# Kernel tuning notes

Measured on AMD Instinct MI355X. Metric: run time of the kernel, lower is better.

Reference implementation:

```python
import jax, jax.numpy as jnp
import numpy as np

EMBED, HEADS, FF, WIN = 512, 8, 2048, 64
SIGMA, PSTRENGTH, PERIOD, THRESH = 2.0, 1.0, 100.0, 0.0


def layer_norm(x, g, b, eps=1e-5):
    mu = jnp.mean(x, axis=-1, keepdims=True)
    var = jnp.var(x, axis=-1, keepdims=True)
    return (x - mu) * jax.lax.rsqrt(var + eps) * g + b


def setup_inputs() -> dict:
    key = jax.random.key(0)
    ks = jax.random.split(key, 16)
    s = 1.0 / np.sqrt(EMBED)
    sf = 1.0 / np.sqrt(FF)
    inp = {
        "src": jax.random.normal(ks[0], (8, 2048, EMBED), dtype=jnp.float32),
        "Wq": jax.random.normal(ks[1], (EMBED, EMBED), dtype=jnp.float32) * s,
        "bq": jnp.zeros((EMBED,), jnp.float32),
        "Wk": jax.random.normal(ks[2], (EMBED, EMBED), dtype=jnp.float32) * s,
        "bk": jnp.zeros((EMBED,), jnp.float32),
        "Wv": jax.random.normal(ks[3], (EMBED, EMBED), dtype=jnp.float32) * s,
        "bv": jnp.zeros((EMBED,), jnp.float32),
        "Wo": jax.random.normal(ks[4], (EMBED, EMBED), dtype=jnp.float32) * s,
        "bo": jnp.zeros((EMBED,), jnp.float32),
        "Wg": jax.random.normal(ks[5], (EMBED, 1), dtype=jnp.float32) * s,
        "bg": jnp.zeros((1,), jnp.float32),
        "W1": jax.random.normal(ks[6], (EMBED, FF), dtype=jnp.float32) * s,
        "b1": jnp.zeros((FF,), jnp.float32),
        "W2": jax.random.normal(ks[7], (FF, EMBED), dtype=jnp.float32) * sf,
        "b2": jnp.zeros((EMBED,), jnp.float32),
        "ln1_g": jnp.ones((EMBED,), jnp.float32),
        "ln1_b": jnp.zeros((EMBED,), jnp.float32),
        "ln2_g": jnp.ones((EMBED,), jnp.float32),
        "ln2_b": jnp.zeros((EMBED,), jnp.float32),
    }
    return inp


def gated_sparse_attn(x, Wq, bq, Wk, bk, Wv, bv, Wo, bo, Wg, bg):
    B, S, D = x.shape
    H, dh = HEADS, D // HEADS
    q = (x @ Wq + bq).reshape(B, S, H, dh).transpose(0, 2, 1, 3)  # [B,H,S,dh]
    k = (x @ Wk + bk).reshape(B, S, H, dh).transpose(0, 2, 1, 3)
    v = (x @ Wv + bv).reshape(B, S, H, dh).transpose(0, 2, 1, 3)
    scores = jnp.einsum('bhqd,bhkd->bhqk', q, k) / jnp.sqrt(jnp.float32(dh))
    idx = jnp.arange(S, dtype=jnp.float32)
    dist = idx[:, None] - idx[None, :]  # [S,S]
    gauss_bias = jnp.exp(-(dist * dist) / (2.0 * SIGMA * SIGMA))
    per_bias = PSTRENGTH * jnp.cos(2.0 * jnp.pi * dist / PERIOD)
    scores = scores + gauss_bias + per_bias  # positional biases baked into scores
    local = jnp.abs(dist) <= WIN  # local-window sparsity mask
    scores = jnp.where(local, scores, jnp.float32(-1e9))
    attn = jax.nn.softmax(scores, axis=-1)
    out = jnp.einsum('bhqk,bhkd->bhqd', attn, v)
    out = out.transpose(0, 2, 1, 3).reshape(B, S, D) @ Wo + bo
    gate = jax.nn.sigmoid(x @ Wg + bg)  # [B,S,1] learned gating
    gate = jnp.where(gate > THRESH, gate, jnp.float32(0.0))
    return gate * out


def reference(src, Wq, bq, Wk, bk, Wv, bv, Wo, bo, Wg, bg, W1, b1, W2, b2, ln1_g, ln1_b, ln2_g, ln2_b):
    # dropout is identity in eval mode
    attn_out = gated_sparse_attn(src, Wq, bq, Wk, bk, Wv, bv, Wo, bo, Wg, bg)
    x = layer_norm(src + attn_out, ln1_g, ln1_b)
    ff = jax.nn.relu(x @ W1 + b1) @ W2 + b2
    return layer_norm(x + ff, ln2_g, ln2_b)
```

## Files before the change

### kernel.cpp

```cpp
#include <hip/hip_runtime.h>
#include <hip/hip_bf16.h>
#include <math.h>

#define S_LEN   2048
#define D_MOD   512
#define N_HEADS 8
#define D_HEAD  64
#define FF_DIM  2048
#define M_ROWS  16384
#define BHSD    8388608

typedef __attribute__((ext_vector_type(8))) __bf16 bf16x8;
typedef __attribute__((ext_vector_type(4))) float  f32x4;
typedef unsigned short u16;

__device__ __forceinline__ u16 f2bf(float f) {
  unsigned u = __float_as_uint(f);
  u += 0x7fffu + ((u >> 16) & 1u);
  return (u16)(u >> 16);
}
__device__ __forceinline__ float bf2f(u16 h) { return __uint_as_float(((unsigned)h) << 16); }

__device__ __forceinline__ f32x4 mfma16(bf16x8 a, bf16x8 b, f32x4 c) {
  return __builtin_amdgcn_mfma_f32_16x16x32_bf16(a, b, c, 0, 0, 0);
}

__device__ __forceinline__ void async16(void* lds, const void* g) {
  __builtin_amdgcn_global_load_lds(
      (const __attribute__((address_space(1))) unsigned int*)g,
      (__attribute__((address_space(3))) unsigned int*)lds, 16, 0, 0);
}

#define BAR()    asm volatile("s_barrier" ::: "memory")
#define WAITV(n) asm volatile("s_waitcnt vmcnt(" #n ")" ::: "memory")
#define WAITL()  asm volatile("s_waitcnt lgkmcnt(0)" ::: "memory")

__device__ __forceinline__ int swz384(int row, int bir) {
  return row * 384 + ((bir & ~127) | ((bir ^ ((row & 7) << 4)) & 127));
}

__global__ __launch_bounds__(256) void cvt_gate(const float* __restrict__ src,
                                                const float* __restrict__ Wg,
                                                const float* __restrict__ bg,
                                                u16* __restrict__ xb,
                                                float* __restrict__ gate) {
  const int wid = threadIdx.x >> 6, lane = threadIdx.x & 63;
  const size_t row = (size_t)blockIdx.x * 4 + wid;
  const float4* s = reinterpret_cast<const float4*>(src + row * D_MOD);
  const float4* w = reinterpret_cast<const float4*>(Wg);
  float4 a0 = s[lane * 2], a1 = s[lane * 2 + 1];
  float4 w0 = w[lane * 2], w1 = w[lane * 2 + 1];
  float acc = a0.x * w0.x + a0.y * w0.y + a0.z * w0.z + a0.w * w0.w +
              a1.x * w1.x + a1.y * w1.y + a1.z * w1.z + a1.w * w1.w;
#pragma unroll
  for (int m = 1; m < 64; m <<= 1) acc += __shfl_xor(acc, m);
  ushort4 h0, h1;
  h0.x = f2bf(a0.x); h0.y = f2bf(a0.y); h0.z = f2bf(a0.z); h0.w = f2bf(a0.w);
  h1.x = f2bf(a1.x); h1.y = f2bf(a1.y); h1.z = f2bf(a1.z); h1.w = f2bf(a1.w);
  ushort4* ob = reinterpret_cast<ushort4*>(xb + row * D_MOD);
  ob[lane * 2] = h0; ob[lane * 2 + 1] = h1;
  if (lane == 0) {
    float g = 1.f / (1.f + __expf(-(acc + bg[0])));
    gate[row] = g > 0.f ? g : 0.f;
  }
}

__global__ void transpose_cvt(const float* __restrict__ in, u16* __restrict__ out,
                              int K, int N) {
  __shared__ float t[32][33];
  const int n0 = blockIdx.x * 32, k0 = blockIdx.y * 32;
  const int tx = threadIdx.x, ty = threadIdx.y;
#pragma unroll
  for (int i = 0; i < 4; ++i)
    t[ty + 8 * i][tx] = in[(size_t)(k0 + ty + 8 * i) * N + n0 + tx];
  __syncthreads();
#pragma unroll
  for (int i = 0; i < 4; ++i)
    out[(size_t)(n0 + ty + 8 * i) * K + k0 + tx] = f2bf(t[tx][ty + 8 * i]);
}

__global__ __launch_bounds__(256) void ln1red_k(const u16* __restrict__ xb,
                                                const float* __restrict__ gate,
                                                const u16* __restrict__ p0,
                                                const u16* __restrict__ p1,
                                                const float* __restrict__ bo,
                                                const float* __restrict__ gam,
                                                const float* __restrict__ bet,
                                                u16* __restrict__ outb) {
  const int wid = threadIdx.x >> 6, lane = threadIdx.x & 63;
  const size_t row = (size_t)blockIdx.x * 4 + wid;
  const size_t base = row * D_MOD;
  const float g = gate[row];
  const ushort4* sp = reinterpret_cast<const ushort4*>(xb + base);
  const ushort4* a  = reinterpret_cast<const ushort4*>(p0 + base);
  const ushort4* c  = reinterpret_cast<const ushort4*>(p1 + base);
  const float4*  bb = reinterpret_cast<const float4*>(bo);
  ushort4 s0 = sp[lane * 2], s1 = sp[lane * 2 + 1];
  ushort4 a0 = a[lane * 2], a1 = a[lane * 2 + 1];
  ushort4 c0 = c[lane * 2], c1 = c[lane * 2 + 1];
  float4 d0 = bb[lane * 2], d1 = bb[lane * 2 + 1];
  float4 v0, v1;
  v0.x = bf2f(s0.x) + g * (bf2f(a0.x) + bf2f(c0.x) + d0.x);
  v0.y = bf2f(s0.y) + g * (bf2f(a0.y) + bf2f(c0.y) + d0.y);
  v0.z = bf2f(s0.z) + g * (bf2f(a0.z) + bf2f(c0.z) + d0.z);
  v0.w = bf2f(s0.w) + g * (bf2f(a0.w) + bf2f(c0.w) + d0.w);
  v1.x = bf2f(s1.x) + g * (bf2f(a1.x) + bf2f(c1.x) + d1.x);
  v1.y = bf2f(s1.y) + g * (bf2f(a1.y) + bf2f(c1.y) + d1.y);
  v1.z = bf2f(s1.z) + g * (bf2f(a1.z) + bf2f(c1.z) + d1.z);
  v1.w = bf2f(s1.w) + g * (bf2f(a1.w) + bf2f(c1.w) + d1.w);
  float s  = v0.x + v0.y + v0.z + v0.w + v1.x + v1.y + v1.z + v1.w;
  float s2 = v0.x * v0.x + v0.y * v0.y + v0.z * v0.z + v0.w * v0.w +
             v1.x * v1.x + v1.y * v1.y + v1.z * v1.z + v1.w * v1.w;
#pragma unroll
  for (int m = 1; m < 64; m <<= 1) { s += __shfl_xor(s, m); s2 += __shfl_xor(s2, m); }
  const float mu = s * (1.0f / 512.0f);
  const float var = s2 * (1.0f / 512.0f) - mu * mu;
  const float rs = 1.0f / sqrtf(var + 1e-5f);
  const float4* gp = reinterpret_cast<const float4*>(gam);
  const float4* bp = reinterpret_cast<const float4*>(bet);
  float4 g0 = gp[lane * 2], g1 = gp[lane * 2 + 1];
  float4 e0 = bp[lane * 2], e1 = bp[lane * 2 + 1];
  ushort4 h0, h1;
  h0.x = f2bf((v0.x - mu) * rs * g0.x + e0.x);  h0.y = f2bf((v0.y - mu) * rs * g0.y + e0.y);
  h0.z = f2bf((v0.z - mu) * rs * g0.z + e0.z);  h0.w = f2bf((v0.w - mu) * rs * g0.w + e0.w);
  h1.x = f2bf((v1.x - mu) * rs * g1.x + e1.x);  h1.y = f2bf((v1.y - mu) * rs * g1.y + e1.y);
  h1.z = f2bf((v1.z - mu) * rs * g1.z + e1.z);  h1.w = f2bf((v1.w - mu) * rs * g1.w + e1.w);
  ushort4* ob = reinterpret_cast<ushort4*>(outb + base);
  ob[lane * 2] = h0; ob[lane * 2 + 1] = h1;
}

__global__ __launch_bounds__(256) void ln2red_k(const u16* __restrict__ xb,
                                                const u16* __restrict__ p0,
                                                const u16* __restrict__ p1,
                                                const float* __restrict__ b2,
                                                const float* __restrict__ gam,
                                                const float* __restrict__ bet,
                                                float* __restrict__ out) {
  const int wid = threadIdx.x >> 6, lane = threadIdx.x & 63;
  const size_t row = (size_t)blockIdx.x * 4 + wid;
  const size_t base = row * D_MOD;
  const ushort4* xp = reinterpret_cast<const ushort4*>(xb + base);
  const ushort4* q0 = reinterpret_cast<const ushort4*>(p0 + base);
  const ushort4* q1 = reinterpret_cast<const ushort4*>(p1 + base);
  const float4* bb = reinterpret_cast<const float4*>(b2);
  ushort4 h0 = xp[lane * 2], h1 = xp[lane * 2 + 1];
  ushort4 a0 = q0[lane * 2], a1 = q0[lane * 2 + 1];
  ushort4 c0 = q1[lane * 2], c1 = q1[lane * 2 + 1];
  float4 d0 = bb[lane * 2], d1 = bb[lane * 2 + 1];
  float4 v0, v1;
  v0.x = bf2f(h0.x) + bf2f(a0.x) + bf2f(c0.x) + d0.x;
  v0.y = bf2f(h0.y) + bf2f(a0.y) + bf2f(c0.y) + d0.y;
  v0.z = bf2f(h0.z) + bf2f(a0.z) + bf2f(c0.z) + d0.z;
  v0.w = bf2f(h0.w) + bf2f(a0.w) + bf2f(c0.w) + d0.w;
  v1.x = bf2f(h1.x) + bf2f(a1.x) + bf2f(c1.x) + d1.x;
  v1.y = bf2f(h1.y) + bf2f(a1.y) + bf2f(c1.y) + d1.y;
  v1.z = bf2f(h1.z) + bf2f(a1.z) + bf2f(c1.z) + d1.z;
  v1.w = bf2f(h1.w) + bf2f(a1.w) + bf2f(c1.w) + d1.w;
  float s  = v0.x + v0.y + v0.z + v0.w + v1.x + v1.y + v1.z + v1.w;
  float s2 = v0.x * v0.x + v0.y * v0.y + v0.z * v0.z + v0.w * v0.w +
             v1.x * v1.x + v1.y * v1.y + v1.z * v1.z + v1.w * v1.w;
#pragma unroll
  for (int m = 1; m < 64; m <<= 1) { s += __shfl_xor(s, m); s2 += __shfl_xor(s2, m); }
  const float mu = s * (1.0f / 512.0f);
  const float var = s2 * (1.0f / 512.0f) - mu * mu;
  const float rs = 1.0f / sqrtf(var + 1e-5f);
  const float4* gp = reinterpret_cast<const float4*>(gam);
  const float4* bp = reinterpret_cast<const float4*>(bet);
  float4 g0 = gp[lane * 2], g1 = gp[lane * 2 + 1];
  float4 e0 = bp[lane * 2], e1 = bp[lane * 2 + 1];
  float4 o0, o1;
  o0.x = (v0.x - mu) * rs * g0.x + e0.x;  o0.y = (v0.y - mu) * rs * g0.y + e0.y;
  o0.z = (v0.z - mu) * rs * g0.z + e0.z;  o0.w = (v0.w - mu) * rs * g0.w + e0.w;
  o1.x = (v1.x - mu) * rs * g1.x + e1.x;  o1.y = (v1.y - mu) * rs * g1.y + e1.y;
  o1.z = (v1.z - mu) * rs * g1.z + e1.z;  o1.w = (v1.w - mu) * rs * g1.w + e1.w;
  float4* q = reinterpret_cast<float4*>(out + base);
  q[lane * 2] = o0; q[lane * 2 + 1] = o1;
}

struct EpiArgs {
  const float* b0; const float* b1; const float* b2;
  float* outf; u16* outb; u16* outb2;
};

template<int EPI, int LD, int NT, int KSLICE, int GX, int GY>
__device__ __forceinline__ void gemm256_body(const u16* __restrict__ A,
                                             const u16* __restrict__ Bt, EpiArgs e) {
  extern __shared__ char smem[];
  char* Asb = smem;
  char* Bsb = smem + 65536;
  const int tid = threadIdx.x;
  const int wid = tid >> 6, lane = tid & 63;
  const int sub = lane >> 4, lc = lane & 15;
  const int wr = wid >> 2, wcn = wid & 3;

  const int nwg = (int)(gridDim.x * gridDim.y * gridDim.z);
  const int orig = ((int)blockIdx.z * (int)gridDim.y + (int)blockIdx.y) * (int)gridDim.x + (int)blockIdx.x;
  const int cpx = nwg >> 3;
  const int wg = (orig & 7) * cpx + (orig >> 3);
  const int bx = wg % GX;
  const int by = (wg / GX) % GY;
  const int bz = wg / (GX * GY);
  const int m0 = by * 256, n0 = bx * 256;
  const int kb = KSLICE * bz;

  const u16* Ab = A + (size_t)m0 * LD;
  const u16* Bb = Bt + (size_t)n0 * LD;

  f32x4 acc[8][4];
#pragma unroll
  for (int i = 0; i < 8; ++i)
#pragma unroll
    for (int j = 0; j < 4; ++j) acc[i][j] = (f32x4){0.f, 0.f, 0.f, 0.f};

  const int lr0 = tid >> 3;
  const int sl  = tid & 7;

#define STAGE(BASE, SRC, BUF, KT)                                              \
  {                                                                            \
    const int kk_ = kb + (KT) * 64;                                            \
    _Pragma("unroll")                                                          \
    for (int r_ = 0; r_ < 4; ++r_) {                                           \
      const int lr_ = r_ * 64 + lr0;                                           \
      async16((BASE) + (BUF) * 32768 + r_ * 8192 + wid * 1024,                 \
              (SRC) + (size_t)lr_ * LD + kk_ + ((sl ^ (lr_ & 7)) << 3));       \
    }                                                                          \
  }
#define LDFRAG(BASE, ROW, KS) \
  (*reinterpret_cast<const bf16x8*>((BASE) + (ROW) * 128 + ((((KS) * 64) + sub * 16) ^ (((ROW) & 7) << 4))))

  STAGE(Bsb, Bb, 0, 0);
  STAGE(Asb, Ab, 0, 0);
  STAGE(Bsb, Bb, 1, 1);
  STAGE(Asb, Ab, 1, 1);
  WAITV(8);
  BAR();

  for (int t = 0; t < NT; ++t) {
    const int buf = t & 1;
    char* Abl = Asb + buf * 32768;
    char* Bbl = Bsb + buf * 32768;
    bf16x8 af[4][2], bfr[2][2][2];
#pragma unroll
    for (int f = 0; f < 4; ++f) {
      const int row = wr * 128 + f * 16 + lc;
#pragma unroll
      for (int ks = 0; ks < 2; ++ks) af[f][ks] = LDFRAG(Abl, row, ks);
    }
#pragma unroll
    for (int f = 0; f < 2; ++f) {
      const int row = wcn * 64 + f * 16 + lc;
#pragma unroll
      for (int ks = 0; ks < 2; ++ks) bfr[0][f][ks] = LDFRAG(Bbl, row, ks);
    }
    __builtin_amdgcn_s_setprio(1);
#pragma unroll
    for (int f = 0; f < 4; ++f)
#pragma unroll
      for (int c = 0; c < 2; ++c)
#pragma unroll
        for (int ks = 0; ks < 2; ++ks)
          acc[f][c] = mfma16(af[f][ks], bfr[0][c][ks], acc[f][c]);
    __builtin_amdgcn_s_setprio(0);
    BAR();
#pragma unroll
    for (int f = 0; f < 2; ++f) {
      const int row = wcn * 64 + 32 + f * 16 + lc;
#pragma unroll
      for (int ks = 0; ks < 2; ++ks) bfr[1][f][ks] = LDFRAG(Bbl, row, ks);
    }
    __builtin_amdgcn_s_setprio(1);
#pragma unroll
    for (int f = 0; f < 4; ++f)
#pragma unroll
      for (int c = 0; c < 2; ++c)
#pragma unroll
        for (int ks = 0; ks < 2; ++ks)
          acc[f][2 + c] = mfma16(af[f][ks], bfr[1][c][ks], acc[f][2 + c]);
    __builtin_amdgcn_s_setprio(0);
    WAITL();
    BAR();
    if (t + 2 < NT) STAGE(Bsb, Bb, buf, t + 2);
#pragma unroll
    for (int f = 0; f < 4; ++f) {
      const int row = wr * 128 + 64 + f * 16 + lc;
#pragma unroll
      for (int ks = 0; ks < 2; ++ks) af[f][ks] = LDFRAG(Abl, row, ks);
    }
    __builtin_amdgcn_s_setprio(1);
#pragma unroll
    for (int f = 0; f < 4; ++f)
#pragma unroll
      for (int c = 0; c < 2; ++c)
#pragma unroll
        for (int ks = 0; ks < 2; ++ks)
          acc[4 + f][2 + c] = mfma16(af[f][ks], bfr[1][c][ks], acc[4 + f][2 + c]);
    __builtin_amdgcn_s_setprio(0);
    WAITL();
    BAR();
    if (t + 2 < NT) STAGE(Asb, Ab, buf, t + 2);
    __builtin_amdgcn_s_setprio(1);
#pragma unroll
    for (int f = 0; f < 4; ++f)
#pragma unroll
      for (int c = 0; c < 2; ++c)
#pragma unroll
        for (int ks = 0; ks < 2; ++ks)
          acc[4 + f][c] = mfma16(af[f][ks], bfr[0][c][ks], acc[4 + f][c]);
    __builtin_amdgcn_s_setprio(0);
    if (t + 1 < NT) {
      if (t + 2 < NT) { WAITV(8); } else { WAITV(0); }
      BAR();
    }
  }
#undef STAGE
#undef LDFRAG

  if constexpr (EPI == 2 || EPI == 4) {
    __syncthreads();
    u16* Cs = reinterpret_cast<u16*>(smem);
#pragma unroll
    for (int fr = 0; fr < 8; ++fr) {
      const int lrow = wr * 128 + fr * 16 + sub * 4;
#pragma unroll
      for (int fc = 0; fc < 4; ++fc) {
        const int lcolb = (wcn * 64 + fc * 16 + lc) * 2;
        float bias = 0.f;
        if constexpr (EPI == 2) bias = e.b0[n0 + wcn * 64 + fc * 16 + lc];
        f32x4 v = acc[fr][fc];
#pragma unroll
        for (int i = 0; i < 4; ++i) {
          float o = v[i] + bias;
          u16 hv;
          if constexpr (EPI == 2) hv = f2bf(o > 0.f ? o : 0.f);
          else                    hv = f2bf(o);
          const int row = lrow + i;
          const int cbs = (lcolb & ~127) | ((lcolb ^ ((row & 7) << 4)) & 127);
          *reinterpret_cast<u16*>((char*)Cs + row * 512 + cbs) = hv;
        }
      }
    }
    __syncthreads();
    u16* dstb;
    size_t pitch;
    if constexpr (EPI == 2) { dstb = e.outb; pitch = FF_DIM; }
    else { dstb = (bz == 0) ? e.outb : e.outb2; pitch = D_MOD; }
#pragma unroll
    for (int p = 0; p < 16; ++p) {
      const int off = p * 8192 + tid * 16;
      const int row = off >> 9, cb = off & 511;
      const int cbs = (cb & ~127) | ((cb ^ ((row & 7) << 4)) & 127);
      uint4 v = *reinterpret_cast<const uint4*>((const char*)Cs + row * 512 + cbs);
      *reinterpret_cast<uint4*>((char*)(dstb + (size_t)(m0 + row) * pitch + n0) + cb) = v;
    }
  } else {
    const int which = n0 >> 9;
    const int bbi = m0 >> 11, ss0 = m0 & 2047;
    if (which == 2) {
      __syncthreads();
      u16* Cs = reinterpret_cast<u16*>(smem);
      const int nnb = n0 & 511;
#pragma unroll
      for (int fr = 0; fr < 8; ++fr) {
        const int lrow = wr * 128 + fr * 16 + sub * 4;
#pragma unroll
        for (int fc = 0; fc < 4; ++fc) {
          const int lcol = wcn * 64 + fc * 16 + lc;
          const float bias = e.b2[nnb + lcol];
          f32x4 v = acc[fr][fc];
#pragma unroll
          for (int i = 0; i < 4; ++i) {
            const int row = lrow + i;
            const int sbyte = (row * 2) ^ ((lcol & 7) << 4);
            *reinterpret_cast<u16*>((char*)Cs + lcol * 512 + sbyte) = f2bf(v[i] + bias);
          }
        }
      }
      __syncthreads();
#pragma unroll
      for (int p = 0; p < 16; ++p) {
        const int off = p * 8192 + tid * 16;
        const int nn = off >> 9, cb = off & 511;
        const int cbs = cb ^ ((nn & 7) << 4);
        uint4 v = *reinterpret_cast<const uint4*>((const char*)Cs + nn * 512 + cbs);
        const int nng = nnb + nn;
        const int hh = nng >> 6, dd = nng & 63;
        *reinterpret_cast<uint4*>(
            (char*)(e.outb2 + (((size_t)bbi * N_HEADS + hh) * D_HEAD + dd) * S_LEN + ss0) + cb) = v;
      }
    } else {
#pragma unroll
      for (int fr = 0; fr < 8; ++fr) {
        const int row0 = m0 + wr * 128 + fr * 16 + sub * 4;
        const int ss = row0 & 2047;
#pragma unroll
        for (int fc = 0; fc < 4; ++fc) {
          const int col = n0 + wcn * 64 + fc * 16 + lc;
          const int nn = col & 511;
          const int hh = nn >> 6, dd = nn & 63;
          const float* bp = (which == 0) ? e.b0 : e.b1;
          const float bias = bp[nn];
          f32x4 v = acc[fr][fc];
#pragma unroll
          for (int i = 0; i < 4; ++i)
            e.outb[(size_t)which * BHSD +
                   (((size_t)bbi * N_HEADS + hh) * S_LEN + ss + i) * D_HEAD + dd]
                = f2bf(v[i] + bias);
        }
      }
    }
  }
}

__global__ __launch_bounds__(512, 2) void k_qkv(const u16* __restrict__ A, const u16* __restrict__ B, EpiArgs e) {
  gemm256_body<0, 512, 8, 0, 6, 64>(A, B, e);
}
__global__ __launch_bounds__(512, 2) void k_ff1(const u16* __restrict__ A, const u16* __restrict__ B, EpiArgs e) {
  gemm256_body<2, 512, 8, 0, 8, 64>(A, B, e);
}
__global__ __launch_bounds__(512, 2) void k_ff2(const u16* __restrict__ A, const u16* __restrict__ B, EpiArgs e) {
  gemm256_body<4, 2048, 16, 1024, 2, 64>(A, B, e);
}
__global__ __launch_bounds__(512, 2) void k_proj(const u16* __restrict__ A, const u16* __restrict__ B, EpiArgs e) {
  gemm256_body<4, 512, 4, 256, 2, 64>(A, B, e);
}

__global__ __launch_bounds__(256)
void attn_k(const u16* __restrict__ Q, const u16* __restrict__ Kt,
            const u16* __restrict__ VTg, u16* __restrict__ Oflat) {
  __shared__ __align__(16) u16 VT[64 * 192];
  __shared__ __align__(16) u16 P [64 * 192];
  __shared__ float tab[256];
  const int tid = threadIdx.x;
  const int wid = tid >> 6, lane = tid & 63;
  const int sub = lane >> 4, lc = lane & 15;
  const int qb = blockIdx.x, bh = blockIdx.y;
  const int bb = bh >> 3, hh = bh & 7;
  const int q0 = qb * 64, kstart = q0 - 64;
  const u16* Qb = Q  + (size_t)bh * S_LEN * D_HEAD;
  const u16* Kb = Kt + (size_t)bh * S_LEN * D_HEAD;
  const u16* Vtb = VTg + (size_t)bh * D_HEAD * S_LEN;

#pragma unroll
  for (int it = 0; it < 6; ++it) {
    const int c = (wid * 6 + it) * 64 + lane;
    const int row = c / 24;
    const int bir = (c % 24) * 16;
    const int swz = (bir & ~127) | ((bir ^ ((row & 7) << 4)) & 127);
    int sb = kstart + (swz >> 1);
    sb = sb < 0 ? 0 : (sb > S_LEN - 8 ? S_LEN - 8 : sb);
    async16((char*)VT + (wid * 6 + it) * 1024, Vtb + (size_t)row * S_LEN + sb);
  }

  if (tid < 255) {
    const int di = tid - 127;
    const float fd = (float)di;
    tab[tid] = (di >= -64 && di <= 64)
        ? __expf(-fd * fd * 0.125f) + __cosf(0.06283185307179586f * fd)
        : -1e9f;
  }

  bf16x8 qf[2];
#pragma unroll
  for (int ks = 0; ks < 2; ++ks)
    qf[ks] = *reinterpret_cast<const bf16x8*>(Qb + (size_t)(q0 + wid * 16 + lc) * D_HEAD + ks * 32 + sub * 8);

  f32x4 sc[12];
#pragma unroll
  for (int t = 0; t < 12; ++t) sc[t] = (f32x4){0.f, 0.f, 0.f, 0.f};
#pragma unroll
  for (int ks = 0; ks < 2; ++ks)
#pragma unroll
    for (int t = 0; t < 12; ++t) {
      int kg = kstart + t * 16 + lc;
      int kc = kg < 0 ? 0 : (kg > S_LEN - 1 ? S_LEN - 1 : kg);
      bf16x8 kf = *reinterpret_cast<const bf16x8*>(Kb + (size_t)kc * D_HEAD + ks * 32 + sub * 8);
      sc[t] = mfma16(qf[ks], kf, sc[t]);
    }
  __syncthreads();

  float rmax[4] = {-3e38f, -3e38f, -3e38f, -3e38f};
#pragma unroll
  for (int t = 0; t < 12; ++t) {
    const int kk = t * 16 + lc;
    const int kg = kstart + kk;
    const bool valid = (kg >= 0) && (kg < S_LEN);
#pragma unroll
    for (int r = 0; r < 4; ++r) {
      const int qrow = wid * 16 + sub * 4 + r;
      const float bias = valid ? tab[qrow - kk + 191] : -1e9f;
      const float sv = sc[t][r] * 0.125f + bias;
      sc[t][r] = sv;
      rmax[r] = fmaxf(rmax[r], sv);
    }
  }
#pragma unroll
  for (int m = 1; m < 16; m <<= 1)
#pragma unroll
    for (int r = 0; r < 4; ++r) rmax[r] = fmaxf(rmax[r], __shfl_xor(rmax[r], m));
  float rsum[4] = {0.f, 0.f, 0.f, 0.f};
#pragma unroll
  for (int t = 0; t < 12; ++t)
#pragma unroll
    for (int r = 0; r < 4; ++r) {
      const float p = __expf(sc[t][r] - rmax[r]);
      sc[t][r] = p; rsum[r] += p;
    }
#pragma unroll
  for (int m = 1; m < 16; m <<= 1)
#pragma unroll
    for (int r = 0; r < 4; ++r) rsum[r] += __shfl_xor(rsum[r], m);
  float rinv[4];
#pragma unroll
  for (int r = 0; r < 4; ++r) rinv[r] = 1.0f / rsum[r];
#pragma unroll
  for (int t = 0; t < 12; ++t)
#pragma unroll
    for (int r = 0; r < 4; ++r) {
      const int qrow = wid * 16 + sub * 4 + r;
      *reinterpret_cast<u16*>(reinterpret_cast<char*>(P) + swz384(qrow, (t * 16 + lc) * 2))
          = f2bf(sc[t][r] * rinv[r]);
    }
  __syncthreads();

  f32x4 oacc[4];
#pragma unroll
  for (int t = 0; t < 4; ++t) oacc[t] = (f32x4){0.f, 0.f, 0.f, 0.f};
  const int arow = wid * 16 + lc;
#pragma unroll
  for (int ks = 0; ks < 6; ++ks) {
    const int bir = ks * 64 + sub * 16;
    bf16x8 pa = *reinterpret_cast<const bf16x8*>(reinterpret_cast<char*>(P) + swz384(arow, bir));
#pragma unroll
    for (int t = 0; t < 4; ++t) {
      bf16x8 vb = *reinterpret_cast<const bf16x8*>(reinterpret_cast<char*>(VT) + swz384(t * 16 + lc, bir));
      oacc[t] = mfma16(pa, vb, oacc[t]);
    }
  }

  const size_t obase = ((size_t)bb * S_LEN + q0) * D_MOD + hh * D_HEAD;
#pragma unroll
  for (int t = 0; t < 4; ++t)
#pragma unroll
    for (int r = 0; r < 4; ++r) {
      const int qrow = wid * 16 + sub * 4 + r;
      Oflat[obase + (size_t)qrow * D_MOD + t * 16 + lc] = f2bf(oacc[t][r]);
    }
}

extern "C" void kernel_launch(void* const* d_in, const int* in_sizes, int n_in,
                              void* d_out, int out_size, void* d_ws, size_t ws_size,
                              hipStream_t stream) {
  (void)in_sizes; (void)n_in; (void)out_size; (void)ws_size;
  const float* src  = (const float*)d_in[0];
  const float* Wq   = (const float*)d_in[1];
  const float* bq   = (const float*)d_in[2];
  const float* Wk   = (const float*)d_in[3];
  const float* bk   = (const float*)d_in[4];
  const float* Wv   = (const float*)d_in[5];
  const float* bv   = (const float*)d_in[6];
  const float* Wo   = (const float*)d_in[7];
  const float* bo   = (const float*)d_in[8];
  const float* Wg   = (const float*)d_in[9];
  const float* bg   = (const float*)d_in[10];
  const float* W1   = (const float*)d_in[11];
  const float* b1   = (const float*)d_in[12];
  const float* W2   = (const float*)d_in[13];
  const float* b2   = (const float*)d_in[14];
  const float* ln1g = (const float*)d_in[15];
  const float* ln1b = (const float*)d_in[16];
  const float* ln2g = (const float*)d_in[17];
  const float* ln2b = (const float*)d_in[18];
  float* out = (float*)d_out;

  char* ws = (char*)d_ws;
  u16*   WqkvT  = (u16*)  (ws + 0);
  u16*   WoT    = (u16*)  (ws + 1572864);
  u16*   W1T    = (u16*)  (ws + 2097152);
  u16*   W2T    = (u16*)  (ws + 4194304);
  float* gatef  = (float*)(ws + 6291456);
  u16*   Xbf    = (u16*)  (ws + 6356992);
  u16*   QKVbf  = (u16*)  (ws + 23134208);
  u16*   attnfl = (u16*)  (ws + 73465856);
  u16*   pr0    = (u16*)  (ws + 90243072);
  u16*   pr1    = (u16*)  (ws + 107020288);
  u16*   xbf2   = (u16*)  (ws + 123797504);
  u16*   VTg    = (u16*)  (ws + 140574720);
  u16*   hbuf   = Xbf;
  u16*   pf0    = pr0;
  u16*   pf1    = pr1;

  (void)hipFuncSetAttribute((const void*)k_qkv,  hipFuncAttributeMaxDynamicSharedMemorySize, 131072);
  (void)hipFuncSetAttribute((const void*)k_ff1,  hipFuncAttributeMaxDynamicSharedMemorySize, 131072);
  (void)hipFuncSetAttribute((const void*)k_ff2,  hipFuncAttributeMaxDynamicSharedMemorySize, 131072);
  (void)hipFuncSetAttribute((const void*)k_proj, hipFuncAttributeMaxDynamicSharedMemorySize, 131072);

  dim3 tb(32, 8);
  cvt_gate<<<4096, 256, 0, stream>>>(src, Wg, bg, Xbf, gatef);
  transpose_cvt<<<dim3(16, 16), tb, 0, stream>>>(Wq, WqkvT,             512, 512);
  transpose_cvt<<<dim3(16, 16), tb, 0, stream>>>(Wk, WqkvT + 512 * 512, 512, 512);
  transpose_cvt<<<dim3(16, 16), tb, 0, stream>>>(Wv, WqkvT + 2 * 512 * 512, 512, 512);
  transpose_cvt<<<dim3(16, 16), tb, 0, stream>>>(Wo, WoT, 512, 512);
  transpose_cvt<<<dim3(64, 16), tb, 0, stream>>>(W1, W1T, 512, 2048);
  transpose_cvt<<<dim3(16, 64), tb, 0, stream>>>(W2, W2T, 2048, 512);

  EpiArgs e1{bq, bk, bv, nullptr, QKVbf, VTg};
  k_qkv<<<dim3(6, 64, 1), 512, 131072, stream>>>(Xbf, WqkvT, e1);

  attn_k<<<dim3(32, 64), 256, 0, stream>>>(QKVbf, QKVbf + BHSD, VTg, attnfl);

  EpiArgs e2{nullptr, nullptr, nullptr, nullptr, pr0, pr1};
  k_proj<<<dim3(2, 64, 2), 512, 131072, stream>>>(attnfl, WoT, e2);

  ln1red_k<<<4096, 256, 0, stream>>>(Xbf, gatef, pr0, pr1, bo, ln1g, ln1b, xbf2);

  EpiArgs e3{b1, nullptr, nullptr, nullptr, hbuf, nullptr};
  k_ff1<<<dim3(8, 64, 1), 512, 131072, stream>>>(xbf2, W1T, e3);

  EpiArgs e4{nullptr, nullptr, nullptr, nullptr, pf0, pf1};
  k_ff2<<<dim3(2, 64, 2), 512, 131072, stream>>>(hbuf, W2T, e4);

  ln2red_k<<<4096, 256, 0, stream>>>(xbf2, pf0, pf1, b2, ln2g, ln2b, out);
}
```

Measured before the change: 224.2 us.

## Simplify GEMM main loop schedule and write epilogue directly to global

```diff
diff --git a/kernel.cpp b/kernel.cpp
--- a/kernel.cpp
+++ b/kernel.cpp
@@ -241,72 +241,44 @@
     char* Bbl = Bsb + buf * 32768;
     bf16x8 af[4][2], bfr[2][2][2];
 #pragma unroll
-    for (int f = 0; f < 4; ++f) {
-      const int row = wr * 128 + f * 16 + lc;
-#pragma unroll
-      for (int ks = 0; ks < 2; ++ks) af[f][ks] = LDFRAG(Abl, row, ks);
-    }
-#pragma unroll
-    for (int f = 0; f < 2; ++f) {
-      const int row = wcn * 64 + f * 16 + lc;
-#pragma unroll
-      for (int ks = 0; ks < 2; ++ks) bfr[0][f][ks] = LDFRAG(Bbl, row, ks);
-    }
+    for (int f = 0; f < 2; ++f)
+#pragma unroll
+      for (int ks = 0; ks < 2; ++ks) {
+        bfr[0][f][ks] = LDFRAG(Bbl, wcn * 64 + f * 16 + lc, ks);
+        bfr[1][f][ks] = LDFRAG(Bbl, wcn * 64 + 32 + f * 16 + lc, ks);
+      }
+#pragma unroll
+    for (int f = 0; f < 4; ++f)
+#pragma unroll
+      for (int ks = 0; ks < 2; ++ks) af[f][ks] = LDFRAG(Abl, wr * 128 + f * 16 + lc, ks);
     __builtin_amdgcn_s_setprio(1);
 #pragma unroll
     for (int f = 0; f < 4; ++f)
 #pragma unroll
-      for (int c = 0; c < 2; ++c)
+      for (int j = 0; j < 4; ++j)
 #pragma unroll
         for (int ks = 0; ks < 2; ++ks)
-          acc[f][c] = mfma16(af[f][ks], bfr[0][c][ks], acc[f][c]);
+          acc[f][j] = mfma16(af[f][ks], bfr[j >> 1][j & 1][ks], acc[f][j]);
     __builtin_amdgcn_s_setprio(0);
-    BAR();
-#pragma unroll
-    for (int f = 0; f < 2; ++f) {
-      const int row = wcn * 64 + 32 + f * 16 + lc;
-#pragma unroll
-      for (int ks = 0; ks < 2; ++ks) bfr[1][f][ks] = LDFRAG(Bbl, row, ks);
-    }
+#pragma unroll
+    for (int f = 0; f < 4; ++f)
+#pragma unroll
+      for (int ks = 0; ks < 2; ++ks) af[f][ks] = LDFRAG(Abl, wr * 128 + 64 + f * 16 + lc, ks);
     __builtin_amdgcn_s_setprio(1);
 #pragma unroll
     for (int f = 0; f < 4; ++f)
 #pragma unroll
-      for (int c = 0; c < 2; ++c)
+      for (int j = 0; j < 4; ++j)
 #pragma unroll
         for (int ks = 0; ks < 2; ++ks)
-          acc[f][2 + c] = mfma16(af[f][ks], bfr[1][c][ks], acc[f][2 + c]);
+          acc[4 + f][j] = mfma16(af[f][ks], bfr[j >> 1][j & 1][ks], acc[4 + f][j]);
     __builtin_amdgcn_s_setprio(0);
     WAITL();
     BAR();
-    if (t + 2 < NT) STAGE(Bsb, Bb, buf, t + 2);
-#pragma unroll
-    for (int f = 0; f < 4; ++f) {
-      const int row = wr * 128 + 64 + f * 16 + lc;
-#pragma unroll
-      for (int ks = 0; ks < 2; ++ks) af[f][ks] = LDFRAG(Abl, row, ks);
-    }
-    __builtin_amdgcn_s_setprio(1);
-#pragma unroll
-    for (int f = 0; f < 4; ++f)
-#pragma unroll
-      for (int c = 0; c < 2; ++c)
-#pragma unroll
-        for (int ks = 0; ks < 2; ++ks)
-          acc[4 + f][2 + c] = mfma16(af[f][ks], bfr[1][c][ks], acc[4 + f][2 + c]);
-    __builtin_amdgcn_s_setprio(0);
-    WAITL();
-    BAR();
-    if (t + 2 < NT) STAGE(Asb, Ab, buf, t + 2);
-    __builtin_amdgcn_s_setprio(1);
-#pragma unroll
-    for (int f = 0; f < 4; ++f)
-#pragma unroll
-      for (int c = 0; c < 2; ++c)
-#pragma unroll
-        for (int ks = 0; ks < 2; ++ks)
-          acc[4 + f][c] = mfma16(af[f][ks], bfr[0][c][ks], acc[4 + f][c]);
-    __builtin_amdgcn_s_setprio(0);
+    if (t + 2 < NT) {
+      STAGE(Bsb, Bb, buf, t + 2);
+      STAGE(Asb, Ab, buf, t + 2);
+    }
     if (t + 1 < NT) {
       if (t + 2 < NT) { WAITV(8); } else { WAITV(0); }
       BAR();
@@ -316,41 +288,26 @@
 #undef LDFRAG
 
   if constexpr (EPI == 2 || EPI == 4) {
-    __syncthreads();
-    u16* Cs = reinterpret_cast<u16*>(smem);
 #pragma unroll
     for (int fr = 0; fr < 8; ++fr) {
-      const int lrow = wr * 128 + fr * 16 + sub * 4;
+      const int row0 = m0 + wr * 128 + fr * 16 + sub * 4;
 #pragma unroll
       for (int fc = 0; fc < 4; ++fc) {
-        const int lcolb = (wcn * 64 + fc * 16 + lc) * 2;
-        float bias = 0.f;
-        if constexpr (EPI == 2) bias = e.b0[n0 + wcn * 64 + fc * 16 + lc];
+        const int col = n0 + wcn * 64 + fc * 16 + lc;
         f32x4 v = acc[fr][fc];
 #pragma unroll
         for (int i = 0; i < 4; ++i) {
-          float o = v[i] + bias;
-          u16 hv;
-          if constexpr (EPI == 2) hv = f2bf(o > 0.f ? o : 0.f);
-          else                    hv = f2bf(o);
-          const int row = lrow + i;
-          const int cbs = (lcolb & ~127) | ((lcolb ^ ((row & 7) << 4)) & 127);
-          *reinterpret_cast<u16*>((char*)Cs + row * 512 + cbs) = hv;
+          const int row = row0 + i;
+          const float val = v[i];
+          if constexpr (EPI == 2) {
+            float o = val + e.b0[col];
+            e.outb[(size_t)row * FF_DIM + col] = f2bf(o > 0.f ? o : 0.f);
+          } else {
+            u16* dst = (bz == 0) ? e.outb : e.outb2;
+            dst[(size_t)row * D_MOD + col] = f2bf(val);
+          }
         }
       }
-    }
-    __syncthreads();
-    u16* dstb;
-    size_t pitch;
-    if constexpr (EPI == 2) { dstb = e.outb; pitch = FF_DIM; }
-    else { dstb = (bz == 0) ? e.outb : e.outb2; pitch = D_MOD; }
-#pragma unroll
-    for (int p = 0; p < 16; ++p) {
-      const int off = p * 8192 + tid * 16;
-      const int row = off >> 9, cb = off & 511;
-      const int cbs = (cb & ~127) | ((cb ^ ((row & 7) << 4)) & 127);
-      uint4 v = *reinterpret_cast<const uint4*>((const char*)Cs + row * 512 + cbs);
-      *reinterpret_cast<uint4*>((char*)(dstb + (size_t)(m0 + row) * pitch + n0) + cb) = v;
     }
   } else {
     const int which = n0 >> 9;
```

Measured after the change: 220.9 us. About the same (-1.5%).
